# Kernel tuning notes

Measured on AMD Instinct MI355X. Metric: run time of the kernel, lower is better.

## Reference

```python
import jax, jax.numpy as jnp
import numpy as np

TEMPERATURE = 0.2
EPS = 1e-12  # matches torch F.normalize eps


def _l2_normalize(x):
    n = jnp.linalg.norm(x, axis=-1, keepdims=True)
    return x / jnp.maximum(n, EPS)


def setup_inputs() -> dict:
    key = jax.random.key(0)
    k1, k2 = jax.random.split(key)
    B, D = 8192, 256
    return {
        "user_embeddings": jax.random.normal(k1, (B, D), dtype=jnp.float32),
        "positive_item_embeddings": jax.random.normal(k2, (B, D), dtype=jnp.float32),
    }


def reference(user_embeddings, positive_item_embeddings):
    # all_item_embeddings=None branch: in-batch implicit negatives.
    u = _l2_normalize(user_embeddings)            # [B, D]
    p = _l2_normalize(positive_item_embeddings)   # [B, D]
    sim = jnp.einsum("bd,nd->bn", u, p) / TEMPERATURE  # [B, B]
    pos_sim = jnp.diagonal(sim)                   # [B]; equals the torch pos_sim
    # Original concatenates pos_sim[i] with the off-diagonal row entries and takes
    # logsumexp. Since the diagonal of sim IS pos_sim[i], that set equals the full
    # row, so loss_i = -pos_sim_i + logsumexp(sim[i, :]). Vectorized over the batch.
    lse = jax.nn.logsumexp(sim, axis=1)           # [B]
    return jnp.mean(lse - pos_sim)
```

## Files before the change

kernel.cpp:

```cpp
#include <hip/hip_runtime.h>
#include <hip/hip_bf16.h>

#define DDIM 256
#define NROWS 8192

typedef __attribute__((ext_vector_type(4))) int int4v;
typedef __attribute__((ext_vector_type(8))) int int8v;
typedef __attribute__((ext_vector_type(16))) float f32x16;

__device__ __forceinline__ void async16(const void* g, void* l) {
    __builtin_amdgcn_global_load_lds(
        (const __attribute__((address_space(1))) unsigned int*)g,
        (__attribute__((address_space(3))) unsigned int*)l,
        16, 0, 0);
}

__device__ __forceinline__ float fexp2(float x) {
    float r; asm("v_exp_f32 %0, %1" : "=v"(r) : "v"(x)); return r;
}

__global__ __launch_bounds__(256) void normalize_kernel(
    const float* __restrict__ U, const float* __restrict__ P,
    unsigned char* __restrict__ Un, unsigned char* __restrict__ Pn,
    float* __restrict__ possim, float* __restrict__ rowsum,
    float* __restrict__ out, int* __restrict__ counter)
{
    if (blockIdx.x == 0 && threadIdx.x == 0) { out[0] = 0.0f; counter[0] = 0; }
    const int tid = threadIdx.x;
    const int row = blockIdx.x * 16 + (tid >> 4);
    const int sl  = tid & 15;
    const float* Ur = U + (size_t)row * DDIM + sl * 16;
    const float* Pr = P + (size_t)row * DDIM + sl * 16;

    float4 u[4], p[4];
    #pragma unroll
    for (int j = 0; j < 4; ++j) {
        u[j] = *(const float4*)(Ur + j * 4);
        p[j] = *(const float4*)(Pr + j * 4);
    }
    float su = 0.0f, sp = 0.0f, up = 0.0f;
    #pragma unroll
    for (int j = 0; j < 4; ++j) {
        su += u[j].x*u[j].x + u[j].y*u[j].y + u[j].z*u[j].z + u[j].w*u[j].w;
        sp += p[j].x*p[j].x + p[j].y*p[j].y + p[j].z*p[j].z + p[j].w*p[j].w;
        up += u[j].x*p[j].x + u[j].y*p[j].y + u[j].z*p[j].z + u[j].w*p[j].w;
    }
    #pragma unroll
    for (int d = 1; d < 16; d <<= 1) {
        su += __shfl_xor(su, d, 16);
        sp += __shfl_xor(sp, d, 16);
        up += __shfl_xor(up, d, 16);
    }
    const float iu = rsqrtf(fmaxf(su, 1e-24f));
    const float ip = rsqrtf(fmaxf(sp, 1e-24f));
    if (sl == 0) {
        possim[row] = up * iu * ip;
        rowsum[row] = 0.0f;
    }
    int4v wu, wp;
    #pragma unroll
    for (int j = 0; j < 4; ++j) {
        unsigned w = (unsigned)__builtin_amdgcn_cvt_pk_fp8_f32(
            u[j].x * iu, u[j].y * iu, 0, false);
        w = (unsigned)__builtin_amdgcn_cvt_pk_fp8_f32(
            u[j].z * iu, u[j].w * iu, (int)w, true);
        wu[j] = (int)w;
        unsigned v = (unsigned)__builtin_amdgcn_cvt_pk_fp8_f32(
            p[j].x * ip, p[j].y * ip, 0, false);
        v = (unsigned)__builtin_amdgcn_cvt_pk_fp8_f32(
            p[j].z * ip, p[j].w * ip, (int)v, true);
        wp[j] = (int)v;
    }
    *(int4v*)(Un + (size_t)row * DDIM + sl * 16) = wu;
    *(int4v*)(Pn + (size_t)row * DDIM + sl * 16) = wp;
}

__global__ __launch_bounds__(512, 2) void sim_exp_rowsum(
    const unsigned char* __restrict__ Un,
    const unsigned char* __restrict__ Pn,
    float* __restrict__ rowsum,
    const float* __restrict__ possim,
    int* __restrict__ counter,
    float* __restrict__ out)
{
    __shared__ __align__(16) unsigned char lds[65536];
    __shared__ float ws8[8];
    __shared__ int ticket_s;

    const int tid  = threadIdx.x;
    const int lane = tid & 63;
    const int wv   = tid >> 6;
    const int m32  = lane & 31;
    const int hi   = lane >> 5;

    const int stripe = blockIdx.x >> 3;
    const int oct    = blockIdx.x & 7;

    const unsigned char* Arow = Un
        + (size_t)(stripe * 256 + wv * 32 + m32) * DDIM + hi * 32;
    union A8 { int8v v; int4v h[2]; };
    A8 afr[4];
    #pragma unroll
    for (int kc = 0; kc < 4; ++kc) {
        afr[kc].h[0] = *(const int4v*)(Arow + kc * 64);
        afr[kc].h[1] = *(const int4v*)(Arow + kc * 64 + 16);
    }

    const int x = m32 & 15, xlo = x & 3;
    const unsigned xh16 = (unsigned)((x & 12) * 16);
    const unsigned bA = (unsigned)(m32 * 256 + (((hi * 2 + 0) ^ xlo) * 16));
    const unsigned bB = (unsigned)(m32 * 256 + (((hi * 2 + 1) ^ xlo) * 16));
    unsigned kterm[4];
    #pragma unroll
    for (int kc = 0; kc < 4; ++kc)
        kterm[kc] = (unsigned)(kc * 64) ^ xh16;

    unsigned soff0, soff1;
    {
        const int r0 = wv * 8 + 0 * 4 + (lane >> 4);
        const int r1 = wv * 8 + 1 * 4 + (lane >> 4);
        const int gp = lane & 15;
        soff0 = (unsigned)(r0 * 256 + ((gp ^ (r0 & 15)) * 16));
        soff1 = (unsigned)(r1 * 256 + ((gp ^ (r1 & 15)) * 16));
    }

    const unsigned char* Bglob = Pn + (size_t)(oct * 1024) * DDIM;

#define STG(T, BUF)                                                          \
    do {                                                                     \
        async16(Bglob + (size_t)(T) * 16384 + soff0,                         \
                lds + (BUF) * 16384 + wv * 2048);                            \
        async16(Bglob + (size_t)(T) * 16384 + soff1,                         \
                lds + (BUF) * 16384 + wv * 2048 + 1024);                     \
    } while (0)

    float rowpart[16];
    #pragma unroll
    for (int g = 0; g < 16; ++g) rowpart[g] = 0.0f;

    STG(0, 0); STG(1, 1); STG(2, 2);
    asm volatile("s_waitcnt vmcnt(0)" ::: "memory");
    __builtin_amdgcn_s_barrier();

    for (int i = 0; i < 16; ++i) {
        if (i > 0) {
            if (i <= 13)      asm volatile("s_waitcnt vmcnt(4)" ::: "memory");
            else if (i == 14) asm volatile("s_waitcnt vmcnt(2)" ::: "memory");
            else              asm volatile("s_waitcnt vmcnt(0)" ::: "memory");
            __builtin_amdgcn_s_barrier();
        }
        if (i + 3 < 16) STG(i + 3, (i + 3) & 3);

        const unsigned char* Bp = lds + (i & 3) * 16384;
        f32x16 acc0, acc1;
        #pragma unroll
        for (int g = 0; g < 16; ++g) { acc0[g] = 0.0f; acc1[g] = 0.0f; }

        #pragma unroll
        for (int kc = 0; kc < 4; ++kc) {
            A8 b0, b1;
            b0.h[0] = *(const int4v*)(Bp + bA + kterm[kc]);
            b0.h[1] = *(const int4v*)(Bp + bB + kterm[kc]);
            b1.h[0] = *(const int4v*)(Bp + bA + kterm[kc] + 8192);
            b1.h[1] = *(const int4v*)(Bp + bB + kterm[kc] + 8192);
            __builtin_amdgcn_s_setprio(1);
            acc0 = __builtin_amdgcn_mfma_scale_f32_32x32x64_f8f6f4(
                afr[kc].v, b0.v, acc0, 0, 0,
                0, 0x7F7F7F7F, 0, 0x7F7F7F7F);
            acc1 = __builtin_amdgcn_mfma_scale_f32_32x32x64_f8f6f4(
                afr[kc].v, b1.v, acc1, 0, 0,
                0, 0x7F7F7F7F, 0, 0x7F7F7F7F);
            __builtin_amdgcn_s_setprio(0);
        }

        #pragma unroll
        for (int g = 0; g < 16; ++g)
            rowpart[g] += fexp2(acc0[g] * 7.2134752044448169f)
                        + fexp2(acc1[g] * 7.2134752044448169f);
    }
#undef STG

    #pragma unroll
    for (int g = 0; g < 16; ++g) {
        float s = rowpart[g];
        s += __shfl_xor(s, 1);
        s += __shfl_xor(s, 2);
        s += __shfl_xor(s, 4);
        s += __shfl_xor(s, 8);
        s += __shfl_xor(s, 16);
        if (m32 == 0) {
            const int grow = stripe * 256 + wv * 32
                           + (g & 3) + 8 * (g >> 2) + 4 * hi;
            atomicAdd(&rowsum[grow], s);
        }
    }

    __threadfence();
    __syncthreads();
    if (tid == 0)
        ticket_s = __hip_atomic_fetch_add(counter, 1, __ATOMIC_ACQ_REL,
                                          __HIP_MEMORY_SCOPE_AGENT);
    __syncthreads();
    if (ticket_s == 255) {
        float part = 0.0f;
        for (int i = tid; i < NROWS; i += 512) {
            const float rs = __hip_atomic_load(&rowsum[i], __ATOMIC_RELAXED,
                                               __HIP_MEMORY_SCOPE_AGENT);
            part += __logf(rs) - 5.0f * possim[i];
        }
        #pragma unroll
        for (int d = 1; d < 64; d <<= 1) part += __shfl_xor(part, d);
        if ((tid & 63) == 0) ws8[wv] = part;
        __syncthreads();
        if (tid == 0) {
            float tot = 0.0f;
            #pragma unroll
            for (int w = 0; w < 8; ++w) tot += ws8[w];
            out[0] = tot * (1.0f / (float)NROWS);
        }
    }
}

extern "C" void kernel_launch(void* const* d_in, const int* in_sizes, int n_in,
                              void* d_out, int out_size, void* d_ws, size_t ws_size,
                              hipStream_t stream) {
    const float* U = (const float*)d_in[0];
    const float* P = (const float*)d_in[1];
    float* out = (float*)d_out;
    char* ws = (char*)d_ws;
    unsigned char* Un = (unsigned char*)ws;
    unsigned char* Pn = (unsigned char*)(ws + 2097152);
    float* rowsum = (float*)(ws + 8388608);
    float* possim = (float*)(ws + 8388608 + 32768);
    int* counter  = (int*)(ws + 8388608 + 65536);

    normalize_kernel<<<NROWS / 16, 256, 0, stream>>>(U, P, Un, Pn, possim, rowsum,
                                                     out, counter);
    sim_exp_rowsum<<<256, 512, 0, stream>>>(Un, Pn, rowsum, possim, counter, out);
}
```

Measured before the change: 129.4 us.

## Double per-warp row tile to reuse each staged B tile across two A blocks

Each warp now holds two 32-row A fragments (64 rows per warp, 512 rows per block), and each block covers 512 columns instead of 1024. Every B tile loaded from LDS therefore feeds four MFMAs instead of two. The aim is to halve LDS reads and global B staging per unit of MFMA work. The cost is higher register pressure from the doubled A fragments and accumulators, which could reduce occupancy under launch bounds (512, 2). The grid stays at 256 blocks.

```diff
diff --git a/kernel.cpp b/kernel.cpp
--- a/kernel.cpp
+++ b/kernel.cpp
@@ -93,17 +93,20 @@
     const int m32  = lane & 31;
     const int hi   = lane >> 5;
 
-    const int stripe = blockIdx.x >> 3;
-    const int oct    = blockIdx.x & 7;
-
-    const unsigned char* Arow = Un
-        + (size_t)(stripe * 256 + wv * 32 + m32) * DDIM + hi * 32;
+    const int stripe = blockIdx.x >> 4;
+    const int cg     = blockIdx.x & 15;
+
     union A8 { int8v v; int4v h[2]; };
-    A8 afr[4];
-    #pragma unroll
-    for (int kc = 0; kc < 4; ++kc) {
-        afr[kc].h[0] = *(const int4v*)(Arow + kc * 64);
-        afr[kc].h[1] = *(const int4v*)(Arow + kc * 64 + 16);
+    A8 afr[2][4];
+    #pragma unroll
+    for (int rb = 0; rb < 2; ++rb) {
+        const unsigned char* Arow = Un
+            + (size_t)(stripe * 512 + wv * 64 + rb * 32 + m32) * DDIM + hi * 32;
+        #pragma unroll
+        for (int kc = 0; kc < 4; ++kc) {
+            afr[rb][kc].h[0] = *(const int4v*)(Arow + kc * 64);
+            afr[rb][kc].h[1] = *(const int4v*)(Arow + kc * 64 + 16);
+        }
     }
 
     const int x = m32 & 15, xlo = x & 3;
@@ -124,7 +127,7 @@
         soff1 = (unsigned)(r1 * 256 + ((gp ^ (r1 & 15)) * 16));
     }
 
-    const unsigned char* Bglob = Pn + (size_t)(oct * 1024) * DDIM;
+    const unsigned char* Bglob = Pn + (size_t)(cg * 512) * DDIM;
 
 #define STG(T, BUF)                                                          \
     do {                                                                     \
@@ -134,27 +137,32 @@
                 lds + (BUF) * 16384 + wv * 2048 + 1024);                     \
     } while (0)
 
-    float rowpart[16];
-    #pragma unroll
-    for (int g = 0; g < 16; ++g) rowpart[g] = 0.0f;
+    float rowpart[2][16];
+    #pragma unroll
+    for (int rb = 0; rb < 2; ++rb)
+        #pragma unroll
+        for (int g = 0; g < 16; ++g) rowpart[rb][g] = 0.0f;
 
     STG(0, 0); STG(1, 1); STG(2, 2);
     asm volatile("s_waitcnt vmcnt(0)" ::: "memory");
     __builtin_amdgcn_s_barrier();
 
-    for (int i = 0; i < 16; ++i) {
+    for (int i = 0; i < 8; ++i) {
         if (i > 0) {
-            if (i <= 13)      asm volatile("s_waitcnt vmcnt(4)" ::: "memory");
-            else if (i == 14) asm volatile("s_waitcnt vmcnt(2)" ::: "memory");
+            if (i <= 5)       asm volatile("s_waitcnt vmcnt(4)" ::: "memory");
+            else if (i == 6)  asm volatile("s_waitcnt vmcnt(2)" ::: "memory");
             else              asm volatile("s_waitcnt vmcnt(0)" ::: "memory");
             __builtin_amdgcn_s_barrier();
         }
-        if (i + 3 < 16) STG(i + 3, (i + 3) & 3);
+        if (i + 3 < 8) STG(i + 3, (i + 3) & 3);
 
         const unsigned char* Bp = lds + (i & 3) * 16384;
-        f32x16 acc0, acc1;
-        #pragma unroll
-        for (int g = 0; g < 16; ++g) { acc0[g] = 0.0f; acc1[g] = 0.0f; }
+        f32x16 acc00, acc01, acc10, acc11;
+        #pragma unroll
+        for (int g = 0; g < 16; ++g) {
+            acc00[g] = 0.0f; acc01[g] = 0.0f;
+            acc10[g] = 0.0f; acc11[g] = 0.0f;
+        }
 
         #pragma unroll
         for (int kc = 0; kc < 4; ++kc) {
@@ -164,34 +172,46 @@
             b1.h[0] = *(const int4v*)(Bp + bA + kterm[kc] + 8192);
             b1.h[1] = *(const int4v*)(Bp + bB + kterm[kc] + 8192);
             __builtin_amdgcn_s_setprio(1);
-            acc0 = __builtin_amdgcn_mfma_scale_f32_32x32x64_f8f6f4(
-                afr[kc].v, b0.v, acc0, 0, 0,
-                0, 0x7F7F7F7F, 0, 0x7F7F7F7F);
-            acc1 = __builtin_amdgcn_mfma_scale_f32_32x32x64_f8f6f4(
-                afr[kc].v, b1.v, acc1, 0, 0,
+            acc00 = __builtin_amdgcn_mfma_scale_f32_32x32x64_f8f6f4(
+                afr[0][kc].v, b0.v, acc00, 0, 0,
+                0, 0x7F7F7F7F, 0, 0x7F7F7F7F);
+            acc01 = __builtin_amdgcn_mfma_scale_f32_32x32x64_f8f6f4(
+                afr[0][kc].v, b1.v, acc01, 0, 0,
+                0, 0x7F7F7F7F, 0, 0x7F7F7F7F);
+            acc10 = __builtin_amdgcn_mfma_scale_f32_32x32x64_f8f6f4(
+                afr[1][kc].v, b0.v, acc10, 0, 0,
+                0, 0x7F7F7F7F, 0, 0x7F7F7F7F);
+            acc11 = __builtin_amdgcn_mfma_scale_f32_32x32x64_f8f6f4(
+                afr[1][kc].v, b1.v, acc11, 0, 0,
                 0, 0x7F7F7F7F, 0, 0x7F7F7F7F);
             __builtin_amdgcn_s_setprio(0);
         }
 
         #pragma unroll
-        for (int g = 0; g < 16; ++g)
-            rowpart[g] += fexp2(acc0[g] * 7.2134752044448169f)
-                        + fexp2(acc1[g] * 7.2134752044448169f);
+        for (int g = 0; g < 16; ++g) {
+            rowpart[0][g] += fexp2(acc00[g] * 7.2134752044448169f)
+                           + fexp2(acc01[g] * 7.2134752044448169f);
+            rowpart[1][g] += fexp2(acc10[g] * 7.2134752044448169f)
+                           + fexp2(acc11[g] * 7.2134752044448169f);
+        }
     }
 #undef STG
 
     #pragma unroll
-    for (int g = 0; g < 16; ++g) {
-        float s = rowpart[g];
-        s += __shfl_xor(s, 1);
-        s += __shfl_xor(s, 2);
-        s += __shfl_xor(s, 4);
-        s += __shfl_xor(s, 8);
-        s += __shfl_xor(s, 16);
-        if (m32 == 0) {
-            const int grow = stripe * 256 + wv * 32
-                           + (g & 3) + 8 * (g >> 2) + 4 * hi;
-            atomicAdd(&rowsum[grow], s);
+    for (int rb = 0; rb < 2; ++rb) {
+        #pragma unroll
+        for (int g = 0; g < 16; ++g) {
+            float s = rowpart[rb][g];
+            s += __shfl_xor(s, 1);
+            s += __shfl_xor(s, 2);
+            s += __shfl_xor(s, 4);
+            s += __shfl_xor(s, 8);
+            s += __shfl_xor(s, 16);
+            if (m32 == 0) {
+                const int grow = stripe * 512 + wv * 64 + rb * 32
+                               + (g & 3) + 8 * (g >> 2) + 4 * hi;
+                atomicAdd(&rowsum[grow], s);
+            }
         }
     }
 
```

Measured after the change: 129.7 us. Within noise of the previous version (+0.3%).
